# Kernel tuning notes

Measured on AMD Instinct MI355X. Metric: run time of the kernel, lower is better.

## Reference

```python
import jax, jax.numpy as jnp
import numpy as np

F0 = 64            # n_filter
NC = 4             # n_calls
NL = 4             # n_layers for image_size=128
CF = 3             # sobel perception factor: [sobel_x, sobel_y, identity]
FIN = F0 * CF      # 192
FH = F0            # 64 hidden
FOUT = 2 * F0      # 128 (gated)
LRELU_SLOPE = 0.2

# constant depthwise kernels (buffers in torch, not trainable)
_gx = np.array([[-1., 0., 1.], [-2., 0., 2.], [-1., 0., 1.]], np.float32) / 8.0
_gy = _gx.T.copy()
_g1 = np.exp(-0.5 * np.array([-1., 0., 1.]) ** 2)
_gk = np.outer(_g1, _g1)
_gk = (_gk / _gk.sum()).astype(np.float32)   # 3x3 gaussian, sigma=1


def _dw3x3(x, k):
    # depthwise 3x3 conv, same kernel per channel, pad=1
    C = x.shape[1]
    kern = jnp.broadcast_to(jnp.asarray(k, x.dtype), (C, 1, 3, 3))
    return jax.lax.conv_general_dilated(
        x, kern, (1, 1), [(1, 1), (1, 1)],
        dimension_numbers=('NCHW', 'OIHW', 'NCHW'), feature_group_count=C)


def _inorm(x, eps=1e-5):
    m = x.mean((2, 3), keepdims=True)
    v = ((x - m) ** 2).mean((2, 3), keepdims=True)
    return (x - m) * jax.lax.rsqrt(v + eps)


def _lrelu(x):
    return jax.nn.leaky_relu(x, LRELU_SLOPE)


def _c11(x, w, b=None):
    # shared 1x1 conv: w [Co,Ci]
    y = jnp.einsum('oi,bihw->bohw', w, x)
    return y if b is None else y + b[None, :, None, None]


def _bc11(x, w, b):
    # per-sample 1x1 conv: w [B,Co,Ci], b [B,Co]
    return jnp.einsum('boi,bihw->bohw', w, x) + b[:, :, None, None]


def _dyna(p, latc, dw, db):
    # hypernetwork: latc [B,512] -> per-sample residual-block 1x1 conv weights
    B = latc.shape[0]
    ks = jnp.einsum('bi,pi->bp', latc, dw) + db
    i0 = FH * FIN; i1 = i0 + FH; i2 = i1 + FOUT * FH
    i3 = i2 + FOUT; i4 = i3 + FOUT * FIN
    w0 = ks[:, :i0].reshape(B, FH, FIN);  b0 = ks[:, i0:i1]
    w1 = ks[:, i1:i2].reshape(B, FOUT, FH); b1 = ks[:, i2:i3]
    ws = ks[:, i3:i4].reshape(B, FOUT, FIN); bs = ks[:, i4:]
    x_s = _bc11(p, ws, bs)
    dx = _bc11(_lrelu(p), w0, b0)
    dx = _bc11(_lrelu(dx), w1, b1)
    return x_s + 0.1 * dx


def _forward(lat, seed, leak_factor, lat_exp_w, lat_exp_b, noise_w,
             dyna_w, dyna_b, conv0_w, conv0_b, conv1_w, conv1_b, convs_w,
             out_w, out_b):
    B = lat.shape[0]
    out = jnp.broadcast_to(seed, (B,) + seed.shape[1:])   # [B,64,16,16]
    lf = jnp.clip(leak_factor, 1e-3, 1e3)
    nkey = jax.random.key(7)
    for c in range(NL * NC):   # 16 structural steps, resolution doubles every NC
        # perception: depthwise sobel + identity -> [B, 3*F0, H, W]
        p = jnp.concatenate([_dw3x3(out, _gx), _dw3x3(out, _gy), out], axis=1)
        p = _inorm(p)
        # shared residual block (1x1 convs)
        xs = _c11(p, convs_w)
        dx = _c11(_lrelu(p), conv0_w, conv0_b)
        dx = _c11(_lrelu(dx), conv1_w, conv1_b)
        f = xs + 0.1 * dx
        # per-step latent expansion (torch Linear: x @ W.T + b)
        latc = jnp.einsum('bi,oi->bo', lat, lat_exp_w[c]) + lat_exp_b[c]
        d = _dyna(p, latc, dyna_w, dyna_b)
        o = f + d                                  # [B, 2*F0, H, W]
        a, g = jnp.split(o, 2, axis=1)
        o = a * jax.nn.sigmoid(g)                  # gated
        # noise injection (stylegan-style, per-channel learned weight)
        noise = jax.random.normal(jax.random.fold_in(nkey, c),
                                  (B, 1) + o.shape[2:], o.dtype)
        o = o + noise_w[c][None, :, None, None] * noise
        out = out + lf * o
        if c < NL * NC - 1 and c % NC == NC - 1:
            Bc, Cc, H, W = out.shape
            out = jax.image.resize(out, (Bc, Cc, 2 * H, 2 * W), method='bilinear')
            out = _dw3x3(out, _gk)                 # gaussian smoothing
    out_raw = _c11(out, out_w, out_b)              # 1x1 out conv -> [B,3,128,128]
    return jnp.clip(out_raw, -1.0, 1.0), out_raw


def setup_inputs() -> dict:
    key = jax.random.key(0)
    ks = jax.random.split(key, 16)
    B, LAT = 8, 512
    P = FH * FIN + FH + FOUT * FH + FOUT + FOUT * FIN + FOUT   # 45376
    r = lambda k, shp, s: jax.random.normal(k, shp, jnp.float32) * s
    return {
        'lat': r(ks[0], (B, LAT), 1.0),
        'seed': r(ks[1], (1, F0, 16, 16), 1.0),
        'leak_factor': jnp.float32(0.1),
        'lat_exp_w': r(ks[2], (NL * NC, LAT, LAT), LAT ** -0.5),
        'lat_exp_b': jnp.zeros((NL * NC, LAT), jnp.float32),
        'noise_w': r(ks[3], (NL * NC, F0), 0.1),
        'dyna_w': r(ks[4], (P, LAT), 2e-3),
        'dyna_b': jnp.zeros((P,), jnp.float32),
        'conv0_w': r(ks[5], (FH, FIN), FIN ** -0.5),
        'conv0_b': jnp.zeros((FH,), jnp.float32),
        'conv1_w': r(ks[6], (FOUT, FH), FH ** -0.5),
        'conv1_b': jnp.zeros((FOUT,), jnp.float32),
        'convs_w': r(ks[7], (FOUT, FIN), FIN ** -0.5),
        'out_w': r(ks[8], (3, F0), F0 ** -0.5),
        'out_b': jnp.zeros((3,), jnp.float32),
    }


def reference(lat, seed, leak_factor, lat_exp_w, lat_exp_b, noise_w,
              dyna_w, dyna_b, conv0_w, conv0_b, conv1_w, conv1_b, convs_w,
              out_w, out_b):
    return _forward(lat, seed, leak_factor, lat_exp_w, lat_exp_b, noise_w,
                    dyna_w, dyna_b, conv0_w, conv0_b, conv1_w, conv1_b,
                    convs_w, out_w, out_b)
```

## Files before the change

### kernel.cpp

```cpp
#include <hip/hip_runtime.h>
#include <cstdint>
#include <cstddef>
#include <cmath>

#define DI __device__ __forceinline__

constexpr int B_ = 8;
constexpr int F0_ = 64;
constexpr int LAT_ = 512;
constexpr int P_ = 45376;
constexpr int NLAY_ = 16;

typedef __attribute__((ext_vector_type(8))) short short8;
typedef __attribute__((ext_vector_type(4))) float f32x4;

constexpr int WPK_STRIDE = 65536;
constexpr int WPK_WS = 24576;
constexpr int WPK_W2 = 49152;

constexpr size_t OFF_PART   = 0;
constexpr size_t OFF_B3     = 24576;
constexpr size_t OFF_LATCBF = 65536;
constexpr size_t OFF_OUT0   = 98304;
constexpr size_t OFF_OUT1   = 8486912;
constexpr size_t OFF_WPK    = 16875520;

DI uint16_t f2bf(float f) {
  uint32_t u = __float_as_uint(f);
  uint32_t r = (u + 0x7FFFu + ((u >> 16) & 1u)) >> 16;
  return (uint16_t)r;
}
DI uint32_t pk2bf(float a, float b) {
  return (uint32_t)f2bf(a) | ((uint32_t)f2bf(b) << 16);
}

DI void tf_cipher(uint32_t k0, uint32_t k1, uint32_t x0, uint32_t x1,
                  uint32_t& o0, uint32_t& o1) {
  const uint32_t ks2 = k0 ^ k1 ^ 0x1BD11BDAu;
  uint32_t a = x0 + k0, b = x1 + k1;
#define TFR(r) { a += b; b = (b << (r)) | (b >> (32 - (r))); b ^= a; }
  TFR(13) TFR(15) TFR(26) TFR(6)  a += k1;  b += ks2 + 1u;
  TFR(17) TFR(29) TFR(16) TFR(24) a += ks2; b += k0 + 2u;
  TFR(13) TFR(15) TFR(26) TFR(6)  a += k0;  b += k1 + 3u;
  TFR(17) TFR(29) TFR(16) TFR(24) a += k1;  b += ks2 + 4u;
  TFR(13) TFR(15) TFR(26) TFR(6)  a += ks2; b += k0 + 5u;
#undef TFR
  o0 = a; o1 = b;
}

static void host_tf_cipher(uint32_t k0, uint32_t k1, uint32_t x0, uint32_t x1,
                           uint32_t& o0, uint32_t& o1) {
  const uint32_t ks2 = k0 ^ k1 ^ 0x1BD11BDAu;
  uint32_t a = x0 + k0, b = x1 + k1;
#define TFR(r) { a += b; b = (b << (r)) | (b >> (32 - (r))); b ^= a; }
  TFR(13) TFR(15) TFR(26) TFR(6)  a += k1;  b += ks2 + 1u;
  TFR(17) TFR(29) TFR(16) TFR(24) a += ks2; b += k0 + 2u;
  TFR(13) TFR(15) TFR(26) TFR(6)  a += k0;  b += k1 + 3u;
  TFR(17) TFR(29) TFR(16) TFR(24) a += k1;  b += ks2 + 4u;
  TFR(13) TFR(15) TFR(26) TFR(6)  a += ks2; b += k0 + 5u;
#undef TFR
  o0 = a; o1 = b;
}

DI float erfinv_f(float x) {
  float w = -log1pf(-x * x);
  float p;
  if (w < 5.0f) {
    w = w - 2.5f;
    p = 2.81022636e-08f;
    p = fmaf(p, w, 3.43273939e-07f);
    p = fmaf(p, w, -3.5233877e-06f);
    p = fmaf(p, w, -4.39150654e-06f);
    p = fmaf(p, w, 0.00021858087f);
    p = fmaf(p, w, -0.00125372503f);
    p = fmaf(p, w, -0.00417768164f);
    p = fmaf(p, w, 0.246640727f);
    p = fmaf(p, w, 1.50140941f);
  } else {
    w = sqrtf(w) - 3.0f;
    p = -0.000200214257f;
    p = fmaf(p, w, 0.000100950558f);
    p = fmaf(p, w, 0.00134934322f);
    p = fmaf(p, w, -0.00367342844f);
    p = fmaf(p, w, 0.00573950773f);
    p = fmaf(p, w, -0.0076224613f);
    p = fmaf(p, w, 0.00943887047f);
    p = fmaf(p, w, 1.00167406f);
    p = fmaf(p, w, 2.83297682f);
  }
  return p * x;
}

DI float noise_val(uint32_t k0, uint32_t k1, uint32_t idx) {
  uint32_t o0, o1;
  tf_cipher(k0, k1, 0u, idx, o0, o1);
  uint32_t bits = o0 ^ o1;
  float f = __uint_as_float((bits >> 9) | 0x3f800000u) - 1.0f;
  const float lo = -0.99999994f;
  float u = fmaxf(lo, fmaf(f, 2.0f, lo));
  return 1.41421354f * erfinv_f(u);
}

__global__ __launch_bounds__(256) void k_seed(const float* __restrict__ seed,
                                              float* __restrict__ outb) {
  const int idx = blockIdx.x * 256 + threadIdx.x;
  const int px = (idx >> 6) & 255, ch = idx & 63;
  outb[idx] = seed[ch * 256 + px];
}

__global__ __launch_bounds__(256) void k_latc(const float* __restrict__ lat,
                                              const float* __restrict__ wexp,
                                              const float* __restrict__ bexp,
                                              unsigned short* __restrict__ latc_bf) {
  const int c = blockIdx.x;
  const int tid = threadIdx.x;
  __shared__ float latS[B_][LAT_];
  for (int i = tid; i < B_ * LAT_; i += 256) latS[i >> 9][i & 511] = lat[i];
  __syncthreads();
  for (int o = tid; o < LAT_; o += 256) {
    float acc[B_] = {0, 0, 0, 0, 0, 0, 0, 0};
    const float* wr = wexp + ((size_t)c * LAT_ + o) * LAT_;
    for (int k = 0; k < LAT_; k += 4) {
      float4 w4 = *(const float4*)(wr + k);
#pragma unroll
      for (int b = 0; b < B_; ++b) {
        acc[b] = fmaf(w4.x, latS[b][k + 0], acc[b]);
        acc[b] = fmaf(w4.y, latS[b][k + 1], acc[b]);
        acc[b] = fmaf(w4.z, latS[b][k + 2], acc[b]);
        acc[b] = fmaf(w4.w, latS[b][k + 3], acc[b]);
      }
    }
    const float bb = bexp[c * LAT_ + o];
#pragma unroll
    for (int b = 0; b < B_; ++b)
      latc_bf[((size_t)c * B_ + b) * LAT_ + o] = f2bf(acc[b] + bb);
  }
}

__global__ __launch_bounds__(256) void k_wstatic(const float* __restrict__ conv0_w,
                                                 const float* __restrict__ conv1_w,
                                                 unsigned short* __restrict__ wpk) {
  const int cb = blockIdx.x;
  unsigned short* wq = wpk + (size_t)cb * WPK_STRIDE;
  for (int i = threadIdx.x; i < 64 * 192; i += 256) wq[i] = f2bf(conv0_w[i]);
  for (int i = threadIdx.x; i < 128 * 64; i += 256) {
    int oc = i >> 6, k = i & 63;
    wq[WPK_W2 + oc * 128 + k] = f2bf(0.1f * conv1_w[i]);
  }
}

__global__ __launch_bounds__(256) void k_ks(
    const unsigned short* __restrict__ latc_bf,
    const float* __restrict__ dyna_w,
    const float* __restrict__ dyna_b,
    const float* __restrict__ convs_w,
    unsigned short* __restrict__ wpk,
    float* __restrict__ bias3) {
  const int n0 = blockIdx.x * 64;
  const int tid = threadIdx.x;
  const int wv = tid >> 6, lane = tid & 63, lg = lane >> 4, lr = lane & 15;
  __shared__ __align__(16) unsigned char AsB[128 * 64];
  __shared__ __align__(16) unsigned char BsB[64 * 64];

  f32x4 acc[2][4];
#pragma unroll
  for (int i = 0; i < 2; ++i)
#pragma unroll
    for (int j = 0; j < 4; ++j) acc[i][j] = (f32x4)0.f;

  const int am = tid >> 1, ah = tid & 1;
  const int bn = tid >> 2, bq = tid & 3;

  for (int kc = 0; kc < LAT_; kc += 32) {
    __syncthreads();
    {
      const uint4* src = (const uint4*)(latc_bf + (size_t)am * LAT_ + kc + ah * 16);
      const uint4 u0 = src[0];
      const uint4 u1 = src[1];
      const int swz = (am & 7) << 4;
      *(uint4*)(AsB + ((am * 64 + ah * 32) ^ swz)) = u0;
      *(uint4*)(AsB + ((am * 64 + ah * 32 + 16) ^ swz)) = u1;
    }
    {
      const float* src = dyna_w + (size_t)(n0 + bn) * LAT_ + kc + bq * 8;
      const float4 f0 = *(const float4*)(src);
      const float4 f1 = *(const float4*)(src + 4);
      uint4 u;
      u.x = pk2bf(f0.x, f0.y);
      u.y = pk2bf(f0.z, f0.w);
      u.z = pk2bf(f1.x, f1.y);
      u.w = pk2bf(f1.z, f1.w);
      *(uint4*)(BsB + ((bn * 64 + bq * 16) ^ ((bn & 7) << 4))) = u;
    }
    __syncthreads();
    short8 af[2], bfx[4];
#pragma unroll
    for (int mt = 0; mt < 2; ++mt) {
      const int rm = wv * 32 + mt * 16 + lr;
      af[mt] = *(const short8*)(AsB + ((rm * 64 + lg * 16) ^ ((rm & 7) << 4)));
    }
#pragma unroll
    for (int nt = 0; nt < 4; ++nt) {
      const int rn = nt * 16 + lr;
      bfx[nt] = *(const short8*)(BsB + ((rn * 64 + lg * 16) ^ ((rn & 7) << 4)));
    }
#pragma unroll
    for (int mt = 0; mt < 2; ++mt)
#pragma unroll
      for (int nt = 0; nt < 4; ++nt)
        acc[mt][nt] = __builtin_amdgcn_mfma_f32_16x16x32_bf16(af[mt], bfx[nt], acc[mt][nt], 0, 0, 0);
  }

#pragma unroll
  for (int nt = 0; nt < 4; ++nt) {
    const int n = n0 + nt * 16 + lr;
    int typ, e_off;
    float addv = 0.f;
    if (n < 12288) { int oc = n / 192; int k = n - oc * 192; typ = 0; e_off = (64 + oc) * 192 + k; }
    else if (n < 12352) { typ = 1; e_off = n - 12288; }
    else if (n < 20544) { int m2 = n - 12352; typ = 2; e_off = WPK_W2 + (m2 >> 6) * 128 + 64 + (m2 & 63); }
    else if (n < 20672) { typ = 3; e_off = 64 + (n - 20544); }
    else if (n < 45248) {
      int m3 = n - 20672; int oc = m3 / 192; int k = m3 - oc * 192;
      typ = 4; e_off = WPK_WS + oc * 192 + k; addv = convs_w[oc * 192 + k];
    } else { typ = 5; e_off = 192 + (n - 45248); }
    const float db = dyna_b[n];
#pragma unroll
    for (int mt = 0; mt < 2; ++mt) {
#pragma unroll
      for (int reg = 0; reg < 4; ++reg) {
        const int cb = wv * 32 + mt * 16 + lg * 4 + reg;
        float v = acc[mt][nt][reg] + db;
        if (typ == 4) v += addv;
        if (typ == 2) v *= 0.1f;
        if (typ == 0 || typ == 2 || typ == 4)
          wpk[(size_t)cb * WPK_STRIDE + e_off] = f2bf(v);
        else
          bias3[(size_t)cb * 320 + e_off] = v;
      }
    }
  }
}

__global__ __launch_bounds__(256) void k_stats1(const float* __restrict__ cur,
                                                float* __restrict__ part,
                                                int H, int W, int logW, int HW) {
  const int b = blockIdx.y;
  const int strip = blockIdx.x;
  const int tid = threadIdx.x;
  const int chq = tid & 15, pxo = (tid >> 4) & 3, wv = tid >> 6;
  const int pxs = HW >> 3;
  const int p0 = strip * pxs;
  const float* __restrict__ ob = cur + (size_t)b * HW * 64 + chq * 4;
  const f32x4 zf = (f32x4)0.f;

  f32x4 s[6];
#pragma unroll
  for (int i = 0; i < 6; ++i) s[i] = zf;

  for (int px = p0 + (wv * 4 + pxo); px < p0 + pxs; px += 16) {
    const int h = px >> logW, w = px & (W - 1);
    const bool vu = h > 0, vd = h < H - 1, vl = w > 0, vr = w < W - 1;
    const float* bp = ob + (size_t)px * 64;
    const int rW = W * 64;
    f32x4 c00 = (vu && vl) ? *(const f32x4*)(bp - rW - 64) : zf;
    f32x4 c01 = vu         ? *(const f32x4*)(bp - rW)      : zf;
    f32x4 c02 = (vu && vr) ? *(const f32x4*)(bp - rW + 64) : zf;
    f32x4 c10 = vl         ? *(const f32x4*)(bp - 64)      : zf;
    f32x4 c11 =              *(const f32x4*)(bp);
    f32x4 c12 = vr         ? *(const f32x4*)(bp + 64)      : zf;
    f32x4 c20 = (vd && vl) ? *(const f32x4*)(bp + rW - 64) : zf;
    f32x4 c21 = vd         ? *(const f32x4*)(bp + rW)      : zf;
    f32x4 c22 = (vd && vr) ? *(const f32x4*)(bp + rW + 64) : zf;
    const f32x4 t0 = c22 - c00, t1 = c02 - c20;
    const f32x4 vx = (t0 + t1 + 2.f * (c12 - c10)) * 0.125f;
    const f32x4 vy = (t0 - t1 + 2.f * (c21 - c01)) * 0.125f;
    s[0] += vx; s[1] += vx * vx;
    s[2] += vy; s[3] += vy * vy;
    s[4] += c11; s[5] += c11 * c11;
  }
#pragma unroll
  for (int i = 0; i < 6; ++i)
#pragma unroll
    for (int c = 0; c < 4; ++c) {
      s[i][c] += __shfl_xor(s[i][c], 16, 64);
      s[i][c] += __shfl_xor(s[i][c], 32, 64);
    }
  __shared__ f32x4 redS[64][6];
  if ((tid & 63) < 16) {
#pragma unroll
    for (int i = 0; i < 6; ++i) redS[wv * 16 + chq][i] = s[i];
  }
  __syncthreads();
  if (tid < 16) {
    f32x4 a[6];
#pragma unroll
    for (int i = 0; i < 6; ++i)
      a[i] = redS[tid][i] + redS[16 + tid][i] + redS[32 + tid][i] + redS[48 + tid][i];
    float* pp = part + (size_t)(b * 8 + strip) * 384;
#pragma unroll
    for (int i = 0; i < 6; ++i) {
      const int sec = i >> 1, wbit = i & 1;
#pragma unroll
      for (int c = 0; c < 4; ++c)
        pp[sec * 128 + wbit * 64 + tid * 4 + c] = a[i][c];
    }
  }
}

__global__ __launch_bounds__(256, 3) void k_main(
    const float* __restrict__ cur, float* __restrict__ nxt,
    const float* __restrict__ part,
    const unsigned short* __restrict__ wpk_layer,
    const float* __restrict__ bias3_layer,
    const float* __restrict__ conv0_b,
    const float* __restrict__ conv1_b,
    const float* __restrict__ noise_w_c,
    const float* __restrict__ leak_ptr,
    int HW, int W, int lwpr, unsigned key0, unsigned key1) {
  const int b = blockIdx.y;
  const int bx = blockIdx.x;
  const int tr = bx >> lwpr, tc = bx & ((1 << lwpr) - 1);
  const int r0 = tr * 4, c0 = tc * 16;
  const int logW = lwpr + 4;
  const int H = HW >> logW;

  const int tid = threadIdx.x;
  const int wv = tid >> 6, lane = tid & 63;
  const int lg = lane >> 4, lr = lane & 15;

  __shared__ __align__(16) unsigned char PrawB[24576];
  __shared__ __align__(16) unsigned char PlreB[24576];
  __shared__ float mrS[384];
  __shared__ float noiseS[64];
  unsigned short* Hs = (unsigned short*)PrawB;

  const unsigned short* wq = wpk_layer + (size_t)b * WPK_STRIDE;
  const unsigned short* W1 = wq;
  const unsigned short* WS = wq + WPK_WS;
  const unsigned short* W2 = wq + WPK_W2;
  const float* b3 = bias3_layer + (size_t)b * 320;

  if (tid < 192) {
    const int sec = tid >> 6, ch = tid & 63;
    const float* pb = part + (size_t)b * 3072;
    float s1 = 0.f, s2 = 0.f;
#pragma unroll
    for (int st = 0; st < 8; ++st) {
      s1 += pb[st * 384 + sec * 128 + ch];
      s2 += pb[st * 384 + sec * 128 + 64 + ch];
    }
    const float inv = 1.0f / (float)HW;
    const float m = s1 * inv;
    mrS[sec * 64 + ch] = m;
    mrS[192 + sec * 64 + ch] = rsqrtf(fmaxf(s2 * inv - m * m, 0.f) + 1e-5f);
  }
  if (tid < 64)
    noiseS[tid] = noise_val(key0, key1,
        (unsigned)(b * HW + (r0 + (tid >> 4)) * W + c0 + (tid & 15)));
  __syncthreads();

  {
    const int pxl = tid & 63;
    const int rl = pxl >> 4, cl = pxl & 15;
    const int gr = r0 + rl, gc = c0 + cl;
    const bool vu = gr > 0, vd = gr < H - 1, vl = gc > 0, vr = gc < W - 1;
    const float* bp = cur + ((size_t)b * HW + (size_t)gr * W + gc) * 64 + wv * 16;
    const int rW = W * 64;
    const f32x4 zf = (f32x4)0.f;
    const int swz = (pxl & 7) << 4;
#pragma unroll
    for (int q = 0; q < 4; ++q) {
      const float* bq = bp + q * 4;
      f32x4 c00 = (vu && vl) ? *(const f32x4*)(bq - rW - 64) : zf;
      f32x4 c01 = vu         ? *(const f32x4*)(bq - rW)      : zf;
      f32x4 c02 = (vu && vr) ? *(const f32x4*)(bq - rW + 64) : zf;
      f32x4 c10 = vl         ? *(const f32x4*)(bq - 64)      : zf;
      f32x4 c11 =              *(const f32x4*)(bq);
      f32x4 c12 = vr         ? *(const f32x4*)(bq + 64)      : zf;
      f32x4 c20 = (vd && vl) ? *(const f32x4*)(bq + rW - 64) : zf;
      f32x4 c21 = vd         ? *(const f32x4*)(bq + rW)      : zf;
      f32x4 c22 = (vd && vr) ? *(const f32x4*)(bq + rW + 64) : zf;
      const f32x4 t0 = c22 - c00, t1 = c02 - c20;
      const f32x4 vx = (t0 + t1 + 2.f * (c12 - c10)) * 0.125f;
      const f32x4 vy = (t0 - t1 + 2.f * (c21 - c01)) * 0.125f;
      const int ch = wv * 16 + q * 4;
      const f32x4 mx = *(const f32x4*)&mrS[ch];
      const f32x4 rx = *(const f32x4*)&mrS[192 + ch];
      const f32x4 my = *(const f32x4*)&mrS[64 + ch];
      const f32x4 ry = *(const f32x4*)&mrS[192 + 64 + ch];
      const f32x4 mi = *(const f32x4*)&mrS[128 + ch];
      const f32x4 ri = *(const f32x4*)&mrS[192 + 128 + ch];
      const f32x4 nx = (vx - mx) * rx;
      const f32x4 ny = (vy - my) * ry;
      const f32x4 ni = (c11 - mi) * ri;
      f32x4 lx, ly, li;
#pragma unroll
      for (int e = 0; e < 4; ++e) {
        lx[e] = fmaxf(nx[e], 0.2f * nx[e]);
        ly[e] = fmaxf(ny[e], 0.2f * ny[e]);
        li[e] = fmaxf(ni[e], 0.2f * ni[e]);
      }
      const int bb = pxl * 384 + ch * 2;
      uint2 u;
      u.x = pk2bf(nx[0], nx[1]); u.y = pk2bf(nx[2], nx[3]);
      *(uint2*)(PrawB + ((bb) ^ swz)) = u;
      u.x = pk2bf(ny[0], ny[1]); u.y = pk2bf(ny[2], ny[3]);
      *(uint2*)(PrawB + ((bb + 128) ^ swz)) = u;
      u.x = pk2bf(ni[0], ni[1]); u.y = pk2bf(ni[2], ni[3]);
      *(uint2*)(PrawB + ((bb + 256) ^ swz)) = u;
      u.x = pk2bf(lx[0], lx[1]); u.y = pk2bf(lx[2], lx[3]);
      *(uint2*)(PlreB + ((bb) ^ swz)) = u;
      u.x = pk2bf(ly[0], ly[1]); u.y = pk2bf(ly[2], ly[3]);
      *(uint2*)(PlreB + ((bb + 128) ^ swz)) = u;
      u.x = pk2bf(li[0], li[1]); u.y = pk2bf(li[2], li[3]);
      *(uint2*)(PlreB + ((bb + 256) ^ swz)) = u;
    }
  }
  __syncthreads();

  const int oc0 = 16 * wv;
  const int oc1 = 64 + 16 * wv;
  f32x4 accH[2][4], accO[2][4];
#pragma unroll
  for (int t = 0; t < 2; ++t)
#pragma unroll
    for (int p = 0; p < 4; ++p) { accH[t][p] = (f32x4)0.f; accO[t][p] = (f32x4)0.f; }

#pragma unroll
  for (int kc = 0; kc < 6; ++kc) {
    const int ko = kc * 32 + lg * 8;
    const short8 a10 = *(const short8*)(W1 + (size_t)(oc0 + lr) * 192 + ko);
    const short8 a11 = *(const short8*)(W1 + (size_t)(oc1 + lr) * 192 + ko);
    const short8 as0 = *(const short8*)(WS + (size_t)(oc0 + lr) * 192 + ko);
    const short8 as1 = *(const short8*)(WS + (size_t)(oc1 + lr) * 192 + ko);
#pragma unroll
    for (int pxt = 0; pxt < 4; ++pxt) {
      const int px = pxt * 16 + lr;
      const int byt = (px * 384 + ko * 2) ^ ((px & 7) << 4);
      const short8 bl = *(const short8*)(PlreB + byt);
      const short8 br = *(const short8*)(PrawB + byt);
      accH[0][pxt] = __builtin_amdgcn_mfma_f32_16x16x32_bf16(a10, bl, accH[0][pxt], 0, 0, 0);
      accH[1][pxt] = __builtin_amdgcn_mfma_f32_16x16x32_bf16(a11, bl, accH[1][pxt], 0, 0, 0);
      accO[0][pxt] = __builtin_amdgcn_mfma_f32_16x16x32_bf16(as0, br, accO[0][pxt], 0, 0, 0);
      accO[1][pxt] = __builtin_amdgcn_mfma_f32_16x16x32_bf16(as1, br, accO[1][pxt], 0, 0, 0);
    }
  }
  __syncthreads();

#pragma unroll
  for (int ti = 0; ti < 2; ++ti) {
    const int ocb = ti ? oc1 : oc0;
    float bh[4];
#pragma unroll
    for (int r = 0; r < 4; ++r) {
      const int oc = ocb + lg * 4 + r;
      bh[r] = (oc < 64) ? conv0_b[oc] : b3[oc - 64];
    }
#pragma unroll
    for (int pxt = 0; pxt < 4; ++pxt) {
      const int px = pxt * 16 + lr;
#pragma unroll
      for (int rp = 0; rp < 2; ++rp) {
        float h0 = accH[ti][pxt][rp * 2 + 0] + bh[rp * 2 + 0];
        float h1 = accH[ti][pxt][rp * 2 + 1] + bh[rp * 2 + 1];
        h0 = fmaxf(h0, 0.2f * h0);
        h1 = fmaxf(h1, 0.2f * h1);
        *(uint32_t*)(&Hs[(size_t)px * 136 + ocb + lg * 4 + rp * 2]) = pk2bf(h0, h1);
      }
    }
  }
  __syncthreads();

#pragma unroll
  for (int kc = 0; kc < 4; ++kc) {
    const int ko = kc * 32 + lg * 8;
    const short8 a20 = *(const short8*)(W2 + (size_t)(oc0 + lr) * 128 + ko);
    const short8 a21 = *(const short8*)(W2 + (size_t)(oc1 + lr) * 128 + ko);
#pragma unroll
    for (int pxt = 0; pxt < 4; ++pxt) {
      const short8 hb = *(const short8*)(&Hs[(size_t)(pxt * 16 + lr) * 136 + ko]);
      accO[0][pxt] = __builtin_amdgcn_mfma_f32_16x16x32_bf16(a20, hb, accO[0][pxt], 0, 0, 0);
      accO[1][pxt] = __builtin_amdgcn_mfma_f32_16x16x32_bf16(a21, hb, accO[1][pxt], 0, 0, 0);
    }
  }

  const float lfv = fminf(fmaxf(leak_ptr[0], 0.001f), 1000.0f);
  float boA[4], boG[4], nw[4];
#pragma unroll
  for (int r = 0; r < 4; ++r) {
    const int oca = oc0 + lg * 4 + r;
    const int ocg = oc1 + lg * 4 + r;
    boA[r] = b3[192 + oca] + 0.1f * (conv1_b[oca] + b3[64 + oca]);
    boG[r] = b3[192 + ocg] + 0.1f * (conv1_b[ocg] + b3[64 + ocg]);
    nw[r] = noise_w_c[oca];
  }
#pragma unroll
  for (int pxt = 0; pxt < 4; ++pxt) {
    const float nz = noiseS[pxt * 16 + lr];
    const size_t adr = ((size_t)b * HW + (size_t)(r0 + pxt) * W + c0 + lr) * 64 + oc0 + lg * 4;
    const f32x4 cv = *(const f32x4*)(cur + adr);
    f32x4 ov;
#pragma unroll
    for (int r = 0; r < 4; ++r) {
      const float a = accO[0][pxt][r] + boA[r];
      const float g = accO[1][pxt][r] + boG[r];
      const float og = a * (1.0f / (1.0f + expf(-g)));
      ov[r] = cv[r] + lfv * (og + nw[r] * nz);
    }
    *(f32x4*)(nxt + adr) = ov;
  }
}

__global__ __launch_bounds__(256) void k_upgauss(const float* __restrict__ src,
                                                 float* __restrict__ dst,
                                                 int H, int W, int loOW, int loOHW,
                                                 float ge, float gm) {
  const int idx = blockIdx.x * 256 + threadIdx.x;
  const int OHW = 1 << loOHW;
  if (idx >= B_ * OHW * 16) return;
  const int chq = idx & 15;
  const int opx = (idx >> 4) & (OHW - 1);
  const int b = idx >> (4 + loOHW);
  const int oh = opx >> loOW, ow = opx & ((1 << loOW) - 1);
  const float g[3] = {ge, gm, ge};

  float wy[3] = {0.f, 0.f, 0.f}, wx[3] = {0.f, 0.f, 0.f};
  const int myi = oh >> 1, mxi = ow >> 1;
#pragma unroll
  for (int d = -1; d <= 1; ++d) {
    {
      const int oo = oh + d;
      if (oo >= 0 && oo < 2 * H) {
        const int i0 = (oo - 1) >> 1;
        const float f = ((oo - 1) & 1) ? 0.75f : 0.25f;
        const int i0c = max(i0, 0), i1c = min(i0 + 1, H - 1);
        wy[i0c - (myi - 1)] += g[d + 1] * (1.f - f);
        wy[i1c - (myi - 1)] += g[d + 1] * f;
      }
    }
    {
      const int oo = ow + d;
      if (oo >= 0 && oo < 2 * W) {
        const int i0 = (oo - 1) >> 1;
        const float f = ((oo - 1) & 1) ? 0.75f : 0.25f;
        const int i0c = max(i0, 0), i1c = min(i0 + 1, W - 1);
        wx[i0c - (mxi - 1)] += g[d + 1] * (1.f - f);
        wx[i1c - (mxi - 1)] += g[d + 1] * f;
      }
    }
  }
  const float* pl = src + ((size_t)b * H * W) * 64 + chq * 4;
  f32x4 acc = (f32x4)0.f;
#pragma unroll
  for (int i = 0; i < 3; ++i) {
    const int ry = min(max(myi - 1 + i, 0), H - 1);
    f32x4 rowv = (f32x4)0.f;
#pragma unroll
    for (int j = 0; j < 3; ++j) {
      const int rx = min(max(mxi - 1 + j, 0), W - 1);
      rowv += wx[j] * *(const f32x4*)(pl + (size_t)(ry * W + rx) * 64);
    }
    acc += wy[i] * rowv;
  }
  *(f32x4*)(dst + ((size_t)b * OHW + opx) * 64 + chq * 4) = acc;
}

__global__ __launch_bounds__(256) void k_final(const float* __restrict__ outbuf,
                                               const float* __restrict__ out_w,
                                               const float* __restrict__ out_b,
                                               float* __restrict__ dout) {
  const int idx = blockIdx.x * 256 + threadIdx.x;
  const int b = idx >> 14, px = idx & 16383;
  const float* src = outbuf + ((size_t)b * 16384 + px) * 64;
  float a0 = out_b[0], a1 = out_b[1], a2 = out_b[2];
  for (int i = 0; i < 64; i += 4) {
    const f32x4 v = *(const f32x4*)(src + i);
    const f32x4 w0 = *(const f32x4*)(out_w + i);
    const f32x4 w1 = *(const f32x4*)(out_w + 64 + i);
    const f32x4 w2 = *(const f32x4*)(out_w + 128 + i);
#pragma unroll
    for (int e = 0; e < 4; ++e) {
      a0 = fmaf(w0[e], v[e], a0);
      a1 = fmaf(w1[e], v[e], a1);
      a2 = fmaf(w2[e], v[e], a2);
    }
  }
  const size_t base = (size_t)b * 49152 + px;
  dout[base] = fminf(fmaxf(a0, -1.f), 1.f);
  dout[base + 16384] = fminf(fmaxf(a1, -1.f), 1.f);
  dout[base + 32768] = fminf(fmaxf(a2, -1.f), 1.f);
  dout[393216 + base] = a0;
  dout[393216 + base + 16384] = a1;
  dout[393216 + base + 32768] = a2;
}

extern "C" void kernel_launch(void* const* d_in, const int* in_sizes, int n_in,
                              void* d_out, int out_size, void* d_ws, size_t ws_size,
                              hipStream_t stream) {
  const float* lat       = (const float*)d_in[0];
  const float* seed      = (const float*)d_in[1];
  const float* leak      = (const float*)d_in[2];
  const float* lat_exp_w = (const float*)d_in[3];
  const float* lat_exp_b = (const float*)d_in[4];
  const float* noise_w   = (const float*)d_in[5];
  const float* dyna_w    = (const float*)d_in[6];
  const float* dyna_b    = (const float*)d_in[7];
  const float* conv0_w   = (const float*)d_in[8];
  const float* conv0_b   = (const float*)d_in[9];
  const float* conv1_w   = (const float*)d_in[10];
  const float* conv1_b   = (const float*)d_in[11];
  const float* convs_w   = (const float*)d_in[12];
  const float* out_w     = (const float*)d_in[13];
  const float* out_b     = (const float*)d_in[14];

  float* wsf = (float*)d_ws;
  float* part = wsf + OFF_PART;
  float* b3   = wsf + OFF_B3;
  unsigned short* latc_bf = (unsigned short*)(wsf + OFF_LATCBF);
  float* out0 = wsf + OFF_OUT0;
  float* out1 = wsf + OFF_OUT1;
  unsigned short* wpk = (unsigned short*)(wsf + OFF_WPK);

  uint32_t lk0[NLAY_], lk1[NLAY_];
  for (int c = 0; c < NLAY_; ++c)
    host_tf_cipher(0u, 7u, 0u, (uint32_t)c, lk0[c], lk1[c]);

  const double ga = exp(-0.5);
  const float ge = (float)(ga / (1.0 + 2.0 * ga));
  const float gm = (float)(1.0 / (1.0 + 2.0 * ga));

  k_seed<<<(B_ * 256 * 64) / 256, 256, 0, stream>>>(seed, out0);
  k_latc<<<NLAY_, 256, 0, stream>>>(lat, lat_exp_w, lat_exp_b, latc_bf);
  k_wstatic<<<NLAY_ * B_, 256, 0, stream>>>(conv0_w, conv1_w, wpk);
  k_ks<<<P_ / 64, 256, 0, stream>>>(latc_bf, dyna_w, dyna_b, convs_w, wpk, b3);

  float* cur = out0;
  float* nxt = out1;
  int H = 16, W = 16, logW = 4;
  for (int c = 0; c < NLAY_; ++c) {
    const int HW = H * W;
    k_stats1<<<dim3(8, B_), 256, 0, stream>>>(cur, part, H, W, logW, HW);
    k_main<<<dim3(HW / 64, B_), 256, 0, stream>>>(
        cur, nxt, part,
        wpk + (size_t)c * B_ * WPK_STRIDE, b3 + (size_t)c * B_ * 320,
        conv0_b, conv1_b, noise_w + c * F0_, leak,
        HW, W, logW - 4, lk0[c], lk1[c]);
    { float* t = cur; cur = nxt; nxt = t; }
    if ((c & 3) == 3 && c < NLAY_ - 1) {
      const int n1 = B_ * 4 * HW * 16;
      const int loOW = logW + 1, loOHW = 2 * logW + 2;
      k_upgauss<<<(n1 + 255) / 256, 256, 0, stream>>>(cur, nxt, H, W, loOW, loOHW, ge, gm);
      { float* t = cur; cur = nxt; nxt = t; }
      H *= 2; W *= 2; logW += 1;
    }
  }
  k_final<<<(B_ * 16384) / 256, 256, 0, stream>>>(cur, out_w, out_b, (float*)d_out);
  (void)in_sizes; (void)n_in; (void)out_size; (void)ws_size;
}
```

Baseline: 1.059 ms.

## Replace leaky-relu input buffer with abs-split GEMM and rescale stats grid

The leaky-relu of the perception input is rewritten as 0.6*x + 0.4*|x|, so the first hidden GEMM runs on the raw bf16 tile twice (once on its sign-cleared copy) with pre-scaled weight copies, and the second 24KB LDS buffer goes away. This frees shared memory, so occupancy is raised to 5 blocks per CU. The stats kernel's strip count now scales with resolution instead of being fixed at 8, and the main kernel's load pattern is remapped to per-row/channel-quad lanes with normalisation constants hoisted. The cost is twice the MFMA work on the hidden GEMM plus a larger weight pack and more workspace.

```diff
diff --git a/kernel.cpp b/kernel.cpp
--- a/kernel.cpp
+++ b/kernel.cpp
@@ -14,16 +14,17 @@
 typedef __attribute__((ext_vector_type(8))) short short8;
 typedef __attribute__((ext_vector_type(4))) float f32x4;
 
-constexpr int WPK_STRIDE = 65536;
-constexpr int WPK_WS = 24576;
-constexpr int WPK_W2 = 49152;
+constexpr int WPK_STRIDE = 90112;
+constexpr int WPK_W1B = 24576;
+constexpr int WPK_WS  = 49152;
+constexpr int WPK_W2  = 73728;
 
 constexpr size_t OFF_PART   = 0;
-constexpr size_t OFF_B3     = 24576;
-constexpr size_t OFF_LATCBF = 65536;
-constexpr size_t OFF_OUT0   = 98304;
-constexpr size_t OFF_OUT1   = 8486912;
-constexpr size_t OFF_WPK    = 16875520;
+constexpr size_t OFF_B3     = 98304;
+constexpr size_t OFF_LATCBF = 139264;
+constexpr size_t OFF_OUT0   = 172032;
+constexpr size_t OFF_OUT1   = 8560640;
+constexpr size_t OFF_WPK    = 16949248;
 
 DI uint16_t f2bf(float f) {
   uint32_t u = __float_as_uint(f);
@@ -142,7 +143,11 @@
                                                  unsigned short* __restrict__ wpk) {
   const int cb = blockIdx.x;
   unsigned short* wq = wpk + (size_t)cb * WPK_STRIDE;
-  for (int i = threadIdx.x; i < 64 * 192; i += 256) wq[i] = f2bf(conv0_w[i]);
+  for (int i = threadIdx.x; i < 64 * 192; i += 256) {
+    const float v = conv0_w[i];
+    wq[i] = f2bf(0.6f * v);
+    wq[WPK_W1B + i] = f2bf(0.4f * v);
+  }
   for (int i = threadIdx.x; i < 128 * 64; i += 256) {
     int oc = i >> 6, k = i & 63;
     wq[WPK_W2 + oc * 128 + k] = f2bf(0.1f * conv1_w[i]);
@@ -233,10 +238,14 @@
         float v = acc[mt][nt][reg] + db;
         if (typ == 4) v += addv;
         if (typ == 2) v *= 0.1f;
-        if (typ == 0 || typ == 2 || typ == 4)
+        if (typ == 0) {
+          wpk[(size_t)cb * WPK_STRIDE + e_off] = f2bf(0.6f * v);
+          wpk[(size_t)cb * WPK_STRIDE + WPK_W1B + e_off] = f2bf(0.4f * v);
+        } else if (typ == 2 || typ == 4) {
           wpk[(size_t)cb * WPK_STRIDE + e_off] = f2bf(v);
-        else
+        } else {
           bias3[(size_t)cb * 320 + e_off] = v;
+        }
       }
     }
   }
@@ -244,12 +253,13 @@
 
 __global__ __launch_bounds__(256) void k_stats1(const float* __restrict__ cur,
                                                 float* __restrict__ part,
-                                                int H, int W, int logW, int HW) {
+                                                int H, int W, int logW, int HW,
+                                                int NS) {
   const int b = blockIdx.y;
   const int strip = blockIdx.x;
   const int tid = threadIdx.x;
   const int chq = tid & 15, pxo = (tid >> 4) & 3, wv = tid >> 6;
-  const int pxs = HW >> 3;
+  const int pxs = HW / NS;
   const int p0 = strip * pxs;
   const float* __restrict__ ob = cur + (size_t)b * HW * 64 + chq * 4;
   const f32x4 zf = (f32x4)0.f;
@@ -297,7 +307,7 @@
 #pragma unroll
     for (int i = 0; i < 6; ++i)
       a[i] = redS[tid][i] + redS[16 + tid][i] + redS[32 + tid][i] + redS[48 + tid][i];
-    float* pp = part + (size_t)(b * 8 + strip) * 384;
+    float* pp = part + (size_t)(b * NS + strip) * 384;
 #pragma unroll
     for (int i = 0; i < 6; ++i) {
       const int sec = i >> 1, wbit = i & 1;
@@ -308,7 +318,7 @@
   }
 }
 
-__global__ __launch_bounds__(256, 3) void k_main(
+__global__ __launch_bounds__(256, 5) void k_main(
     const float* __restrict__ cur, float* __restrict__ nxt,
     const float* __restrict__ part,
     const unsigned short* __restrict__ wpk_layer,
@@ -317,7 +327,7 @@
     const float* __restrict__ conv1_b,
     const float* __restrict__ noise_w_c,
     const float* __restrict__ leak_ptr,
-    int HW, int W, int lwpr, unsigned key0, unsigned key1) {
+    int HW, int W, int lwpr, int NS, unsigned key0, unsigned key1) {
   const int b = blockIdx.y;
   const int bx = blockIdx.x;
   const int tr = bx >> lwpr, tc = bx & ((1 << lwpr) - 1);
@@ -330,23 +340,22 @@
   const int lg = lane >> 4, lr = lane & 15;
 
   __shared__ __align__(16) unsigned char PrawB[24576];
-  __shared__ __align__(16) unsigned char PlreB[24576];
   __shared__ float mrS[384];
   __shared__ float noiseS[64];
   unsigned short* Hs = (unsigned short*)PrawB;
 
   const unsigned short* wq = wpk_layer + (size_t)b * WPK_STRIDE;
-  const unsigned short* W1 = wq;
-  const unsigned short* WS = wq + WPK_WS;
-  const unsigned short* W2 = wq + WPK_W2;
+  const unsigned short* W1A = wq;
+  const unsigned short* W1B = wq + WPK_W1B;
+  const unsigned short* WS  = wq + WPK_WS;
+  const unsigned short* W2  = wq + WPK_W2;
   const float* b3 = bias3_layer + (size_t)b * 320;
 
   if (tid < 192) {
     const int sec = tid >> 6, ch = tid & 63;
-    const float* pb = part + (size_t)b * 3072;
+    const float* pb = part + (size_t)b * NS * 384;
     float s1 = 0.f, s2 = 0.f;
-#pragma unroll
-    for (int st = 0; st < 8; ++st) {
+    for (int st = 0; st < NS; ++st) {
       s1 += pb[st * 384 + sec * 128 + ch];
       s2 += pb[st * 384 + sec * 128 + 64 + ch];
     }
@@ -361,17 +370,25 @@
   __syncthreads();
 
   {
-    const int pxl = tid & 63;
-    const int rl = pxl >> 4, cl = pxl & 15;
-    const int gr = r0 + rl, gc = c0 + cl;
-    const bool vu = gr > 0, vd = gr < H - 1, vl = gc > 0, vr = gc < W - 1;
-    const float* bp = cur + ((size_t)b * HW + (size_t)gr * W + gc) * 64 + wv * 16;
+    const int pxi = lane >> 4;
+    const int chq = lane & 15;
+    const int ch = chq * 4;
+    const int gr = r0 + wv;
+    const bool vu = gr > 0, vd = gr < H - 1;
     const int rW = W * 64;
     const f32x4 zf = (f32x4)0.f;
-    const int swz = (pxl & 7) << 4;
-#pragma unroll
-    for (int q = 0; q < 4; ++q) {
-      const float* bq = bp + q * 4;
+    const f32x4 mx = *(const f32x4*)&mrS[ch];
+    const f32x4 rx = *(const f32x4*)&mrS[192 + ch];
+    const f32x4 my = *(const f32x4*)&mrS[64 + ch];
+    const f32x4 ry = *(const f32x4*)&mrS[192 + 64 + ch];
+    const f32x4 mi = *(const f32x4*)&mrS[128 + ch];
+    const f32x4 ri = *(const f32x4*)&mrS[192 + 128 + ch];
+#pragma unroll
+    for (int it = 0; it < 4; ++it) {
+      const int cl = it * 4 + pxi;
+      const int gc = c0 + cl;
+      const bool vl = gc > 0, vr = gc < W - 1;
+      const float* bq = cur + ((size_t)b * HW + (size_t)gr * W + gc) * 64 + ch;
       f32x4 c00 = (vu && vl) ? *(const f32x4*)(bq - rW - 64) : zf;
       f32x4 c01 = vu         ? *(const f32x4*)(bq - rW)      : zf;
       f32x4 c02 = (vu && vr) ? *(const f32x4*)(bq - rW + 64) : zf;
@@ -384,23 +401,11 @@
       const f32x4 t0 = c22 - c00, t1 = c02 - c20;
       const f32x4 vx = (t0 + t1 + 2.f * (c12 - c10)) * 0.125f;
       const f32x4 vy = (t0 - t1 + 2.f * (c21 - c01)) * 0.125f;
-      const int ch = wv * 16 + q * 4;
-      const f32x4 mx = *(const f32x4*)&mrS[ch];
-      const f32x4 rx = *(const f32x4*)&mrS[192 + ch];
-      const f32x4 my = *(const f32x4*)&mrS[64 + ch];
-      const f32x4 ry = *(const f32x4*)&mrS[192 + 64 + ch];
-      const f32x4 mi = *(const f32x4*)&mrS[128 + ch];
-      const f32x4 ri = *(const f32x4*)&mrS[192 + 128 + ch];
       const f32x4 nx = (vx - mx) * rx;
       const f32x4 ny = (vy - my) * ry;
       const f32x4 ni = (c11 - mi) * ri;
-      f32x4 lx, ly, li;
-#pragma unroll
-      for (int e = 0; e < 4; ++e) {
-        lx[e] = fmaxf(nx[e], 0.2f * nx[e]);
-        ly[e] = fmaxf(ny[e], 0.2f * ny[e]);
-        li[e] = fmaxf(ni[e], 0.2f * ni[e]);
-      }
+      const int pxl = wv * 16 + cl;
+      const int swz = (pxl & 7) << 4;
       const int bb = pxl * 384 + ch * 2;
       uint2 u;
       u.x = pk2bf(nx[0], nx[1]); u.y = pk2bf(nx[2], nx[3]);
@@ -409,12 +414,6 @@
       *(uint2*)(PrawB + ((bb + 128) ^ swz)) = u;
       u.x = pk2bf(ni[0], ni[1]); u.y = pk2bf(ni[2], ni[3]);
       *(uint2*)(PrawB + ((bb + 256) ^ swz)) = u;
-      u.x = pk2bf(lx[0], lx[1]); u.y = pk2bf(lx[2], lx[3]);
-      *(uint2*)(PlreB + ((bb) ^ swz)) = u;
-      u.x = pk2bf(ly[0], ly[1]); u.y = pk2bf(ly[2], ly[3]);
-      *(uint2*)(PlreB + ((bb + 128) ^ swz)) = u;
-      u.x = pk2bf(li[0], li[1]); u.y = pk2bf(li[2], li[3]);
-      *(uint2*)(PlreB + ((bb + 256) ^ swz)) = u;
     }
   }
   __syncthreads();
@@ -430,20 +429,24 @@
 #pragma unroll
   for (int kc = 0; kc < 6; ++kc) {
     const int ko = kc * 32 + lg * 8;
-    const short8 a10 = *(const short8*)(W1 + (size_t)(oc0 + lr) * 192 + ko);
-    const short8 a11 = *(const short8*)(W1 + (size_t)(oc1 + lr) * 192 + ko);
-    const short8 as0 = *(const short8*)(WS + (size_t)(oc0 + lr) * 192 + ko);
-    const short8 as1 = *(const short8*)(WS + (size_t)(oc1 + lr) * 192 + ko);
+    const short8 a1a0 = *(const short8*)(W1A + (size_t)(oc0 + lr) * 192 + ko);
+    const short8 a1a1 = *(const short8*)(W1A + (size_t)(oc1 + lr) * 192 + ko);
+    const short8 a1b0 = *(const short8*)(W1B + (size_t)(oc0 + lr) * 192 + ko);
+    const short8 a1b1 = *(const short8*)(W1B + (size_t)(oc1 + lr) * 192 + ko);
+    const short8 as0  = *(const short8*)(WS + (size_t)(oc0 + lr) * 192 + ko);
+    const short8 as1  = *(const short8*)(WS + (size_t)(oc1 + lr) * 192 + ko);
 #pragma unroll
     for (int pxt = 0; pxt < 4; ++pxt) {
       const int px = pxt * 16 + lr;
       const int byt = (px * 384 + ko * 2) ^ ((px & 7) << 4);
-      const short8 bl = *(const short8*)(PlreB + byt);
       const short8 br = *(const short8*)(PrawB + byt);
-      accH[0][pxt] = __builtin_amdgcn_mfma_f32_16x16x32_bf16(a10, bl, accH[0][pxt], 0, 0, 0);
-      accH[1][pxt] = __builtin_amdgcn_mfma_f32_16x16x32_bf16(a11, bl, accH[1][pxt], 0, 0, 0);
+      const short8 babs = br & (short)0x7FFF;
       accO[0][pxt] = __builtin_amdgcn_mfma_f32_16x16x32_bf16(as0, br, accO[0][pxt], 0, 0, 0);
       accO[1][pxt] = __builtin_amdgcn_mfma_f32_16x16x32_bf16(as1, br, accO[1][pxt], 0, 0, 0);
+      accH[0][pxt] = __builtin_amdgcn_mfma_f32_16x16x32_bf16(a1a0, br, accH[0][pxt], 0, 0, 0);
+      accH[1][pxt] = __builtin_amdgcn_mfma_f32_16x16x32_bf16(a1a1, br, accH[1][pxt], 0, 0, 0);
+      accH[0][pxt] = __builtin_amdgcn_mfma_f32_16x16x32_bf16(a1b0, babs, accH[0][pxt], 0, 0, 0);
+      accH[1][pxt] = __builtin_amdgcn_mfma_f32_16x16x32_bf16(a1b1, babs, accH[1][pxt], 0, 0, 0);
     }
   }
   __syncthreads();
@@ -640,12 +643,13 @@
   int H = 16, W = 16, logW = 4;
   for (int c = 0; c < NLAY_; ++c) {
     const int HW = H * W;
-    k_stats1<<<dim3(8, B_), 256, 0, stream>>>(cur, part, H, W, logW, HW);
+    const int NS = (HW >= 16384) ? 32 : ((HW >= 4096) ? 8 : ((HW >= 1024) ? 4 : 1));
+    k_stats1<<<dim3(NS, B_), 256, 0, stream>>>(cur, part, H, W, logW, HW, NS);
     k_main<<<dim3(HW / 64, B_), 256, 0, stream>>>(
         cur, nxt, part,
         wpk + (size_t)c * B_ * WPK_STRIDE, b3 + (size_t)c * B_ * 320,
         conv0_b, conv1_b, noise_w + c * F0_, leak,
-        HW, W, logW - 4, lk0[c], lk1[c]);
+        HW, W, logW - 4, NS, lk0[c], lk1[c]);
     { float* t = cur; cur = nxt; nxt = t; }
     if ((c & 3) == 3 && c < NLAY_ - 1) {
       const int n1 = B_ * 4 * HW * 16;
```

After: 1.441 ms. +36.1%, slower.
